# Kernel optimization log

Hardware: AMD Instinct MI355X
Metric: run time of the kernel (lower is better)

The kernel has to match this reference:

```python
import jax, jax.numpy as jnp
import numpy as np
from jax import lax

B, C, H, W = 8, 64, 256, 256
WSIZES = [8, 8]
DRATES = [1, 2]
SHIFT = True
CS = C // len(WSIZES)          # split channels = 32
SCALE = CS ** (-0.5)
EPS = 1e-6


def _ln2d(x, w, b):
    # channel-wise LayerNorm over dim 1 (biased variance), per LayerNormFunction
    mu = x.mean(1, keepdims=True)
    var = ((x - mu) ** 2).mean(1, keepdims=True)
    y = (x - mu) / jnp.sqrt(var + EPS)
    return w[None, :, None, None] * y + b[None, :, None, None]


def _conv1d(x, w, pad, dil):
    # x: [b, ci, L], w: [co, ci, k]
    return lax.conv_general_dilated(x, w, (1,), ((pad, pad),), rhs_dilation=(dil,),
                                    dimension_numbers=('NCH', 'OIH', 'NCH'))


def _eca(x, w1, w2, w3, wc):
    # x: [b,c,h,w] -> channel attention [b,c,1,1]
    y = x.mean((2, 3))[:, None, :]                      # [b,1,c]
    y1 = _conv1d(y, w1, 1, 1)
    y2 = _conv1d(y, w2, 2, 2)
    y3 = _conv1d(y, w3, 4, 4)
    y = _conv1d(jnp.concatenate([y1, y2, y3], axis=1), wc, 1, 1)  # [b,1,c]
    return jax.nn.sigmoid(jnp.transpose(y, (0, 2, 1))[..., None])  # [b,c,1,1]


def _conv1x1(x, w):
    # w: [co, ci]
    return jnp.einsum('bchw,oc->bohw', x, w)


def _win(x, ws):
    # [b,c,H,W] -> [(b nh nw), ws*ws, c]
    b, c, h, w = x.shape
    nh, nw = h // ws, w // ws
    x = x.reshape(b, c, nh, ws, nw, ws).transpose(0, 2, 4, 3, 5, 1)
    return x.reshape(b * nh * nw, ws * ws, c)


def _unwin(x, b, nh, nw, ws):
    c = x.shape[-1]
    x = x.reshape(b, nh, nw, ws, ws, c).transpose(0, 5, 1, 3, 2, 4)
    return x.reshape(b, c, nh * ws, nw * ws)


def setup_inputs() -> dict:
    key = jax.random.key(0)
    ks = jax.random.split(key, 16)
    g = lambda k, shape: jax.random.normal(k, shape, jnp.float32) * 0.02
    return {
        'x0': jax.random.normal(ks[0], (B, C, H, W), jnp.float32),
        'ln_w': jnp.ones((C,), jnp.float32),
        'ln_b': jnp.zeros((C,), jnp.float32),
        'dw_w': g(ks[1], (C, 1, 3, 3)),
        'dw_b': jnp.zeros((C,), jnp.float32),
        'eca_w1': g(ks[2], (1, 1, 3)),
        'eca_w2': g(ks[3], (1, 1, 3)),
        'eca_w3': g(ks[4], (1, 1, 3)),
        'eca_wc': g(ks[5], (1, 3, 3)),
        'wq': g(ks[6], (C, C)),
        'wk': g(ks[7], (C, C)),
        'wv': g(ks[8], (C, C)),
        'down_w': g(ks[9], (CS, 1, 2, 2)),
        'down_b': jnp.zeros((CS,), jnp.float32),
        'sa_w': g(ks[10], (1, C)),
        'sa_b': jnp.zeros((1,), jnp.float32),
        'po_w': g(ks[11], (C, C)),
        'po_b': jnp.zeros((C,), jnp.float32),
    }


def reference(x0, ln_w, ln_b, dw_w, dw_b, eca_w1, eca_w2, eca_w3, eca_wc,
              wq, wk, wv, down_w, down_b, sa_w, sa_b, po_w, po_b):
    b, c, h, w = x0.shape
    x = _ln2d(x0, ln_w, ln_b)
    # depthwise 3x3
    x1 = lax.conv_general_dilated(x, dw_w, (1, 1), ((1, 1), (1, 1)),
                                  feature_group_count=c,
                                  dimension_numbers=('NCHW', 'OIHW', 'NCHW'))
    x1 = x1 + dw_b[None, :, None, None]
    ca = _eca(x1, eca_w1, eca_w2, eca_w3, eca_wc)
    vs = jnp.split(_conv1x1(x, wv) * ca, len(WSIZES), axis=1)
    qs = jnp.split(_conv1x1(x, wq), len(WSIZES), axis=1)
    ks_ = jnp.split(_conv1x1(x, wk), len(WSIZES), axis=1)

    ys = []
    for idx in range(len(WSIZES)):
        ws = WSIZES[idx]
        ds = ws // DRATES[idx]
        q = qs[idx]
        if SHIFT:
            q = jnp.roll(q, (-ws // 2, -ws // 2), (2, 3))
        q = _win(q, ws)
        if DRATES[idx] != 1:
            # depthwise 2x2 stride-2 downsample of k, v
            def down(t):
                t = lax.conv_general_dilated(t, down_w, (2, 2), 'VALID',
                                             feature_group_count=CS,
                                             dimension_numbers=('NCHW', 'OIHW', 'NCHW'))
                return t + down_b[None, :, None, None]
            k = down(ks_[idx])
            v = down(vs[idx])
            if SHIFT:
                k = jnp.roll(k, (-ds // 2, -ds // 2), (2, 3))
                v = jnp.roll(v, (-ds // 2, -ds // 2), (2, 3))
            k = _win(k, ds)
            v = _win(v, ds)
        else:
            k, v = ks_[idx], vs[idx]
            if SHIFT:
                k = jnp.roll(k, (-ws // 2, -ws // 2), (2, 3))
                v = jnp.roll(v, (-ws // 2, -ws // 2), (2, 3))
            k = _win(k, ws)
            v = _win(v, ws)
        atn = jax.nn.softmax(jnp.einsum('nqc,nkc->nqk', q, k) * SCALE, axis=-1)
        y_ = jnp.einsum('nqk,nkc->nqc', atn, v)
        y_ = _unwin(y_, b, h // ws, w // ws, ws)
        if SHIFT:
            y_ = jnp.roll(y_, (ws // 2, ws // 2), (2, 3))
        ys.append(y_)

    y = jnp.concatenate(ys, axis=1)
    x1m = jax.nn.sigmoid(_conv1x1(y, sa_w) + sa_b[None, :, None, None]) * x1
    y = _conv1x1(y + x1m, po_w) + po_b[None, :, None, None]
    return y + x0
```

## Files before the change

kernel.cpp:

```cpp
#include <hip/hip_runtime.h>
#include <hip/hip_bf16.h>

using bf16 = __hip_bfloat16;

constexpr int B = 8, C = 64, H = 256, W = 256;
constexpr int HWs = H * W;
constexpr int NPIX = B * H * W;
constexpr long long NELEM = (long long)B * C * H * W;
constexpr int CS = 32;
constexpr int Hd = 128, Wd = 128;
constexpr int HWd = Hd * Wd;
constexpr int NDOWN = B * CS * HWd;
constexpr float EPS = 1e-6f;
constexpr float SCALE = 0.17677669529663687f;

typedef __attribute__((ext_vector_type(8))) short short8v;
typedef __attribute__((ext_vector_type(8))) unsigned short ushort8v;
typedef __attribute__((ext_vector_type(4))) unsigned short ushort4v;
typedef __attribute__((ext_vector_type(4))) float f32x4;

__device__ __forceinline__ float b2f(bf16 v) { return __bfloat162float(v); }
__device__ __forceinline__ bf16 f2b(float v) { return __float2bfloat16(v); }
__device__ __forceinline__ unsigned short f2bu(float v) {
  bf16 t = __float2bfloat16(v);
  unsigned short u;
  __builtin_memcpy(&u, &t, 2);
  return u;
}
__device__ __forceinline__ float bu2f(unsigned short u) {
  bf16 t;
  __builtin_memcpy(&t, &u, 2);
  return __bfloat162float(t);
}
__device__ __forceinline__ short8v pack2(ushort4v a, ushort4v b) {
  short8v r;
  r[0] = (short)a[0]; r[1] = (short)a[1]; r[2] = (short)a[2]; r[3] = (short)a[3];
  r[4] = (short)b[0]; r[5] = (short)b[1]; r[6] = (short)b[2]; r[7] = (short)b[3];
  return r;
}

__global__ __launch_bounds__(256) void qkv_ln_kernel(
    const float* __restrict__ x0, const float* __restrict__ lnw,
    const float* __restrict__ lnb, const float* __restrict__ wq,
    const float* __restrict__ wk, const float* __restrict__ wv,
    unsigned short* __restrict__ xo, unsigned short* __restrict__ q0,
    unsigned short* __restrict__ q1, unsigned short* __restrict__ k0,
    unsigned short* __restrict__ v0, unsigned short* __restrict__ ksp,
    unsigned short* __restrict__ vsp) {
  __shared__ unsigned short sA[4][2560];
  __shared__ unsigned short sB[4][2560];
  int lane = threadIdx.x & 63, wid = threadIdx.x >> 6;
  int lr = lane & 15, lg = lane >> 4;
  unsigned short* A = &sA[wid][0];
  unsigned short* Bs = &sB[wid][0];
  int seg = blockIdx.x * 4 + wid;
  int p0 = seg * 64;
  int b = p0 >> 16;
  int hw0 = p0 & (HWs - 1);
  int r = hw0 >> 8, col0 = hw0 & 255;
  float lwv[16], lbv[16];
#pragma unroll
  for (int ks = 0; ks < 2; ++ks)
#pragma unroll
    for (int j = 0; j < 8; ++j) {
      int c = ks * 32 + lg * 4 + (j & 3) + 16 * (j >> 2);
      lwv[ks * 8 + j] = lnw[c];
      lbv[ks * 8 + j] = lnb[c];
    }
  short8v bx[4][2];
#pragma unroll
  for (int st = 0; st < 4; ++st) {
    const float* xp = x0 + (size_t)b * C * HWs + hw0 + st * 16 + lr;
    float xv[16];
#pragma unroll
    for (int ks = 0; ks < 2; ++ks)
#pragma unroll
      for (int j = 0; j < 8; ++j) {
        int c = ks * 32 + lg * 4 + (j & 3) + 16 * (j >> 2);
        xv[ks * 8 + j] = xp[(size_t)c * HWs];
      }
    float s = 0.f, s2 = 0.f;
#pragma unroll
    for (int i = 0; i < 16; ++i) { s += xv[i]; s2 += xv[i] * xv[i]; }
    s += __shfl_xor(s, 16, 64); s += __shfl_xor(s, 32, 64);
    s2 += __shfl_xor(s2, 16, 64); s2 += __shfl_xor(s2, 32, 64);
    float mu = s * (1.f / 64);
    float var = s2 * (1.f / 64) - mu * mu;
    float rstd = rsqrtf(var + EPS);
#pragma unroll
    for (int ks = 0; ks < 2; ++ks)
#pragma unroll
      for (int j = 0; j < 8; ++j) {
        float xn = lwv[ks * 8 + j] * ((xv[ks * 8 + j] - mu) * rstd) + lbv[ks * 8 + j];
        bx[st][ks][j] = (short)f2bu(xn);
      }
  }
  int rr = (r - 4) & 255;
  int tokr = (rr & 7) * 8;
  int wrow = b * 1024 + (rr >> 3) * 32;
  auto win_store = [&](const unsigned short* src, unsigned short* dst) {
#pragma unroll
    for (int i = 0; i < 4; ++i) {
      int g = i * 4 + (lane >> 4);
      int tl = (lane >> 2) & 3, ch8 = lane & 3;
      int px = g * 4 + tl;
      int ccw = (col0 + px - 4) & 255;
      size_t wb = (size_t)(wrow + (ccw >> 3)) * 2048 +
                  (size_t)(tokr + (ccw & 7)) * 32 + ch8 * 8;
      ushort8v d = *(const ushort8v*)(src + px * 40 + ch8 * 8);
      *(ushort8v*)(dst + wb) = d;
    }
  };
  auto load_wfrag = [&](const float* wsrc, short8v wf[4][2]) {
#pragma unroll
    for (int mt = 0; mt < 4; ++mt)
#pragma unroll
      for (int ks = 0; ks < 2; ++ks) {
        int rowoff = (mt * 16 + lr) * 64 + ks * 32 + lg * 4;
        short8v t;
#pragma unroll
        for (int j = 0; j < 8; ++j) {
          int kj = (j & 3) + 16 * (j >> 2);
          t[j] = (short)f2bu(wsrc[rowoff + kj]);
        }
        wf[mt][ks] = t;
      }
  };
  f32x4 zero = {0.f, 0.f, 0.f, 0.f};
#pragma unroll
  for (int half = 0; half < 2; ++half) {
#pragma unroll
    for (int st = 0; st < 4; ++st) {
      int px = st * 16 + lr;
#pragma unroll
      for (int j = 0; j < 8; ++j) {
        int c = lg * 4 + (j & 3) + 16 * (j >> 2);
        Bs[c * 80 + px] = (unsigned short)bx[st][half][j];
      }
    }
#pragma unroll
    for (int i = 0; i < 4; ++i) {
      int ch = i * 8 + (lane >> 3), pxg = lane & 7;
      ushort8v d = *(const ushort8v*)(Bs + ch * 80 + pxg * 8);
      *(ushort8v*)(xo + ((size_t)b * 64 + half * 32 + ch) * HWs + hw0 + pxg * 8) = d;
    }
  }
  {
    short8v wf[4][2];
    load_wfrag(wq, wf);
#pragma unroll
    for (int st = 0; st < 4; ++st) {
      f32x4 acc[4];
#pragma unroll
      for (int mt = 0; mt < 4; ++mt) {
        acc[mt] = __builtin_amdgcn_mfma_f32_16x16x32_bf16(wf[mt][0], bx[st][0], zero, 0, 0, 0);
        acc[mt] = __builtin_amdgcn_mfma_f32_16x16x32_bf16(wf[mt][1], bx[st][1], acc[mt], 0, 0, 0);
      }
      int px = st * 16 + lr;
#pragma unroll
      for (int mt = 0; mt < 2; ++mt)
#pragma unroll
        for (int i = 0; i < 4; ++i)
          A[px * 40 + mt * 16 + lg * 4 + i] = f2bu(acc[mt][i]);
#pragma unroll
      for (int mt = 2; mt < 4; ++mt)
#pragma unroll
        for (int i = 0; i < 4; ++i)
          Bs[px * 40 + (mt - 2) * 16 + lg * 4 + i] = f2bu(acc[mt][i]);
    }
    win_store(A, q0);
    win_store(Bs, q1);
  }
  {
    short8v wf[4][2];
    load_wfrag(wk, wf);
#pragma unroll
    for (int st = 0; st < 4; ++st) {
      f32x4 acc[4];
#pragma unroll
      for (int mt = 0; mt < 4; ++mt) {
        acc[mt] = __builtin_amdgcn_mfma_f32_16x16x32_bf16(wf[mt][0], bx[st][0], zero, 0, 0, 0);
        acc[mt] = __builtin_amdgcn_mfma_f32_16x16x32_bf16(wf[mt][1], bx[st][1], acc[mt], 0, 0, 0);
      }
      int px = st * 16 + lr;
#pragma unroll
      for (int mt = 0; mt < 2; ++mt)
#pragma unroll
        for (int i = 0; i < 4; ++i)
          A[px * 40 + mt * 16 + lg * 4 + i] = f2bu(acc[mt][i]);
#pragma unroll
      for (int mt = 2; mt < 4; ++mt)
#pragma unroll
        for (int i = 0; i < 4; ++i)
          Bs[((mt - 2) * 16 + lg * 4 + i) * 80 + px] = f2bu(acc[mt][i]);
    }
    win_store(A, k0);
#pragma unroll
    for (int i = 0; i < 4; ++i) {
      int ch = i * 8 + (lane >> 3), pxg = lane & 7;
      ushort8v d = *(const ushort8v*)(Bs + ch * 80 + pxg * 8);
      *(ushort8v*)(ksp + ((size_t)b * 32 + ch) * HWs + hw0 + pxg * 8) = d;
    }
  }
  {
    short8v wf[4][2];
    load_wfrag(wv, wf);
#pragma unroll
    for (int st = 0; st < 4; ++st) {
      f32x4 acc[4];
#pragma unroll
      for (int mt = 0; mt < 4; ++mt) {
        acc[mt] = __builtin_amdgcn_mfma_f32_16x16x32_bf16(wf[mt][0], bx[st][0], zero, 0, 0, 0);
        acc[mt] = __builtin_amdgcn_mfma_f32_16x16x32_bf16(wf[mt][1], bx[st][1], acc[mt], 0, 0, 0);
      }
      int px = st * 16 + lr;
#pragma unroll
      for (int mt = 0; mt < 2; ++mt)
#pragma unroll
        for (int i = 0; i < 4; ++i)
          A[px * 40 + mt * 16 + lg * 4 + i] = f2bu(acc[mt][i]);
#pragma unroll
      for (int mt = 2; mt < 4; ++mt)
#pragma unroll
        for (int i = 0; i < 4; ++i)
          Bs[((mt - 2) * 16 + lg * 4 + i) * 80 + px] = f2bu(acc[mt][i]);
    }
    win_store(A, v0);
#pragma unroll
    for (int i = 0; i < 4; ++i) {
      int ch = i * 8 + (lane >> 3), pxg = lane & 7;
      ushort8v d = *(const ushort8v*)(Bs + ch * 80 + pxg * 8);
      *(ushort8v*)(vsp + ((size_t)b * 32 + ch) * HWs + hw0 + pxg * 8) = d;
    }
  }
}

__global__ __launch_bounds__(256) void dw_kernel(
    const unsigned short* __restrict__ x, const float* __restrict__ dww,
    const float* __restrict__ dwb, unsigned short* __restrict__ x1,
    float* __restrict__ pool) {
  int tid = threadIdx.x;
  int tx = tid & 15, ty = tid >> 4;
  int h = blockIdx.x * 16 + ty;
  int c = blockIdx.y, b = blockIdx.z;
  const unsigned short* xp = x + ((size_t)b * C + c) * HWs;
  float kk[9];
#pragma unroll
  for (int i = 0; i < 9; ++i) kk[i] = dww[c * 9 + i];
  int w0 = tx * 16;
  float acc[16];
  float bias = dwb[c];
#pragma unroll
  for (int i = 0; i < 16; ++i) acc[i] = bias;
#pragma unroll
  for (int dr = 0; dr < 3; ++dr) {
    int hh = h + dr - 1;
    if (hh < 0 || hh >= H) continue;
    const unsigned short* rp = xp + hh * W;
    ushort8v r0 = *(const ushort8v*)(rp + w0);
    ushort8v r1 = *(const ushort8v*)(rp + w0 + 8);
    float p[18];
    p[0] = (w0 > 0) ? bu2f(rp[w0 - 1]) : 0.f;
    p[17] = (w0 + 16 < W) ? bu2f(rp[w0 + 16]) : 0.f;
#pragma unroll
    for (int i = 0; i < 8; ++i) { p[1 + i] = bu2f(r0[i]); p[9 + i] = bu2f(r1[i]); }
    float k0 = kk[dr * 3], k1 = kk[dr * 3 + 1], k2 = kk[dr * 3 + 2];
#pragma unroll
    for (int i = 0; i < 16; ++i)
      acc[i] += k0 * p[i] + k1 * p[i + 1] + k2 * p[i + 2];
  }
  ushort8v o0, o1;
  float s = 0.f;
#pragma unroll
  for (int i = 0; i < 8; ++i) { o0[i] = f2bu(acc[i]); o1[i] = f2bu(acc[i + 8]); }
#pragma unroll
  for (int i = 0; i < 16; ++i) s += acc[i];
  size_t ob = ((size_t)b * C + c) * HWs + h * W + w0;
  *(ushort8v*)(x1 + ob) = o0;
  *(ushort8v*)(x1 + ob + 8) = o1;
#pragma unroll
  for (int off = 32; off > 0; off >>= 1) s += __shfl_down(s, off, 64);
  __shared__ float red[4];
  if ((tid & 63) == 0) red[tid >> 6] = s;
  __syncthreads();
  if (tid == 0) atomicAdd(&pool[b * C + c], red[0] + red[1] + red[2] + red[3]);
}

__global__ __launch_bounds__(512) void eca_kernel(
    const float* __restrict__ pool, const float* __restrict__ w1,
    const float* __restrict__ w2, const float* __restrict__ w3,
    const float* __restrict__ wc, float* __restrict__ ca) {
  int tid = threadIdx.x;
  int b = tid >> 6, c = tid & 63;
  __shared__ float m[8][64], t1[8][64], t2[8][64], t3[8][64];
  m[b][c] = pool[tid] * (1.f / HWs);
  __syncthreads();
  auto gm = [&](int cc) -> float { return (cc >= 0 && cc < 64) ? m[b][cc] : 0.f; };
  t1[b][c] = w1[0] * gm(c - 1) + w1[1] * gm(c) + w1[2] * gm(c + 1);
  t2[b][c] = w2[0] * gm(c - 2) + w2[1] * gm(c) + w2[2] * gm(c + 2);
  t3[b][c] = w3[0] * gm(c - 4) + w3[1] * gm(c) + w3[2] * gm(c + 4);
  __syncthreads();
  auto g1 = [&](int cc) -> float { return (cc >= 0 && cc < 64) ? t1[b][cc] : 0.f; };
  auto g2 = [&](int cc) -> float { return (cc >= 0 && cc < 64) ? t2[b][cc] : 0.f; };
  auto g3 = [&](int cc) -> float { return (cc >= 0 && cc < 64) ? t3[b][cc] : 0.f; };
  float z = 0.f;
#pragma unroll
  for (int k = 0; k < 3; ++k) {
    z += wc[0 * 3 + k] * g1(c + k - 1);
    z += wc[1 * 3 + k] * g2(c + k - 1);
    z += wc[2 * 3 + k] * g3(c + k - 1);
  }
  ca[tid] = 1.f / (1.f + __expf(-z));
}

__global__ __launch_bounds__(256) void down_kernel(
    const unsigned short* __restrict__ ksp, const unsigned short* __restrict__ vsp,
    const float* __restrict__ dw, const float* __restrict__ db,
    unsigned short* __restrict__ kdw, unsigned short* __restrict__ vdw) {
  int t = blockIdx.x * 256 + threadIdx.x;
  int wxd = t & 31, i = (t >> 5) & 127, c = (t >> 12) & 31, b = t >> 17;
  const unsigned short* kp = ksp + ((size_t)b * 32 + c) * HWs;
  const unsigned short* vp = vsp + ((size_t)b * 32 + c) * HWs;
  float w00 = dw[c * 4], w01 = dw[c * 4 + 1], w10 = dw[c * 4 + 2], w11 = dw[c * 4 + 3];
  float bias = db[c];
  int rowa = (2 * i) * W, rowb = rowa + W;
  int c0a = (8 * wxd + 4) & 255, c0b = (8 * wxd + 8) & 255;
  ushort4v ka0 = *(const ushort4v*)(kp + rowa + c0a);
  ushort4v ka1 = *(const ushort4v*)(kp + rowa + c0b);
  ushort4v kb0 = *(const ushort4v*)(kp + rowb + c0a);
  ushort4v kb1 = *(const ushort4v*)(kp + rowb + c0b);
  ushort4v va0 = *(const ushort4v*)(vp + rowa + c0a);
  ushort4v va1 = *(const ushort4v*)(vp + rowa + c0b);
  ushort4v vb0 = *(const ushort4v*)(vp + rowb + c0a);
  ushort4v vb1 = *(const ushort4v*)(vp + rowb + c0b);
  int rr = (i - 2) & 127;
  size_t winb = ((size_t)(b * 1024 + (rr >> 2) * 32 + wxd)) * 512;
  int tokrow = (rr & 3) * 4;
  ushort4v hk, hv;
#pragma unroll
  for (int tx = 0; tx < 4; ++tx) {
    float k00, k01, k10, k11, v00, v01, v10, v11;
    if (tx < 2) {
      k00 = bu2f(ka0[2 * tx]); k01 = bu2f(ka0[2 * tx + 1]);
      k10 = bu2f(kb0[2 * tx]); k11 = bu2f(kb0[2 * tx + 1]);
      v00 = bu2f(va0[2 * tx]); v01 = bu2f(va0[2 * tx + 1]);
      v10 = bu2f(vb0[2 * tx]); v11 = bu2f(vb0[2 * tx + 1]);
    } else {
      k00 = bu2f(ka1[2 * (tx - 2)]); k01 = bu2f(ka1[2 * (tx - 2) + 1]);
      k10 = bu2f(kb1[2 * (tx - 2)]); k11 = bu2f(kb1[2 * (tx - 2) + 1]);
      v00 = bu2f(va1[2 * (tx - 2)]); v01 = bu2f(va1[2 * (tx - 2) + 1]);
      v10 = bu2f(vb1[2 * (tx - 2)]); v11 = bu2f(vb1[2 * (tx - 2) + 1]);
    }
    hk[tx] = f2bu(w00 * k00 + w01 * k01 + w10 * k10 + w11 * k11 + bias);
    hv[tx] = f2bu(w00 * v00 + w01 * v01 + w10 * v10 + w11 * v11 + bias);
  }
  *(ushort4v*)(vdw + winb + (size_t)c * 16 + tokrow) = hv;
#pragma unroll
  for (int tx = 0; tx < 4; ++tx)
    kdw[winb + (size_t)(tokrow + tx) * 32 + c] = hk[tx];
}

__global__ __launch_bounds__(256) void attn0_kernel(
    const unsigned short* __restrict__ q0, const unsigned short* __restrict__ k0,
    const unsigned short* __restrict__ v0, const float* __restrict__ ca,
    unsigned short* __restrict__ y) {
  __shared__ unsigned short zs[4][32][72];
  int tid = threadIdx.x;
  int lane = tid & 63, wid = tid >> 6;
  int lr = lane & 15, lg = lane >> 4;
  int widx = blockIdx.x * 4 + wid;
  int b = widx >> 10;
  unsigned short* zw = &zs[wid][0][0];
  float cav[8];
#pragma unroll
  for (int mt = 0; mt < 2; ++mt)
#pragma unroll
    for (int r2 = 0; r2 < 4; ++r2)
      cav[mt * 4 + r2] = ca[b * 64 + mt * 16 + lg * 4 + r2];
  {
    const unsigned short* vp = v0 + (size_t)widx * 2048 + (size_t)lane * 32;
#pragma unroll
    for (int j2 = 0; j2 < 4; ++j2) {
      ushort8v vv = *(const ushort8v*)(vp + j2 * 8);
#pragma unroll
      for (int i = 0; i < 8; ++i) zw[(j2 * 8 + i) * 72 + lane] = vv[i];
    }
  }
  const unsigned short* kw = k0 + (size_t)widx * 2048;
  const unsigned short* qw = q0 + (size_t)widx * 2048;
  short8v kf[4], qf[4];
#pragma unroll
  for (int kt = 0; kt < 4; ++kt) {
    ushort4v a = *(const ushort4v*)(kw + (kt * 16 + lr) * 32 + lg * 4);
    ushort4v b2 = *(const ushort4v*)(kw + (kt * 16 + lr) * 32 + lg * 4 + 16);
    kf[kt] = pack2(a, b2);
  }
#pragma unroll
  for (int qt = 0; qt < 4; ++qt) {
    ushort4v a = *(const ushort4v*)(qw + (qt * 16 + lr) * 32 + lg * 4);
    ushort4v b2 = *(const ushort4v*)(qw + (qt * 16 + lr) * 32 + lg * 4 + 16);
    qf[qt] = pack2(a, b2);
  }
  __syncthreads();
  short8v va[2][2];
#pragma unroll
  for (int mt = 0; mt < 2; ++mt)
#pragma unroll
    for (int ck = 0; ck < 2; ++ck) {
      ushort4v a = *(const ushort4v*)&zw[(mt * 16 + lr) * 72 + ck * 32 + lg * 4];
      ushort4v b2 = *(const ushort4v*)&zw[(mt * 16 + lr) * 72 + ck * 32 + lg * 4 + 16];
      va[mt][ck] = pack2(a, b2);
    }
  f32x4 zero = {0.f, 0.f, 0.f, 0.f};
#pragma unroll
  for (int qt = 0; qt < 4; ++qt) {
    f32x4 st[4];
#pragma unroll
    for (int kt = 0; kt < 4; ++kt)
      st[kt] = __builtin_amdgcn_mfma_f32_16x16x32_bf16(kf[kt], qf[qt], zero, 0, 0, 0);
    float mx = -1e30f;
#pragma unroll
    for (int kt = 0; kt < 4; ++kt)
#pragma unroll
      for (int r2 = 0; r2 < 4; ++r2) mx = fmaxf(mx, st[kt][r2]);
    mx = fmaxf(mx, __shfl_xor(mx, 16, 64));
    mx = fmaxf(mx, __shfl_xor(mx, 32, 64));
    float sum = 0.f;
#pragma unroll
    for (int kt = 0; kt < 4; ++kt)
#pragma unroll
      for (int r2 = 0; r2 < 4; ++r2) {
        float e = __expf(SCALE * (st[kt][r2] - mx));
        st[kt][r2] = e;
        sum += e;
      }
    sum += __shfl_xor(sum, 16, 64);
    sum += __shfl_xor(sum, 32, 64);
    float inv = 1.f / sum;
    short8v pb[2];
#pragma unroll
    for (int ck = 0; ck < 2; ++ck)
#pragma unroll
      for (int j = 0; j < 8; ++j)
        pb[ck][j] = (short)f2bu(st[ck * 2 + (j >> 2)][j & 3]);
#pragma unroll
    for (int mt = 0; mt < 2; ++mt) {
      f32x4 yt = __builtin_amdgcn_mfma_f32_16x16x32_bf16(va[mt][0], pb[0], zero, 0, 0, 0);
      yt = __builtin_amdgcn_mfma_f32_16x16x32_bf16(va[mt][1], pb[1], yt, 0, 0, 0);
#pragma unroll
      for (int r2 = 0; r2 < 4; ++r2)
        zw[(mt * 16 + lg * 4 + r2) * 72 + qt * 16 + lr] = f2bu(yt[r2] * inv * cav[mt * 4 + r2]);
    }
  }
  __syncthreads();
  int widx0 = blockIdx.x * 4;
  int b0 = widx0 >> 10, wy0 = (widx0 >> 5) & 31, wxb = widx0 & 31;
#pragma unroll
  for (int pass = 0; pass < 4; ++pass) {
    int sub = tid & 3, pair = tid >> 2;
    int ch = pair & 31;
    int row = pass * 2 + (pair >> 5);
    ushort8v t8 = *(const ushort8v*)&zs[sub][ch][row * 8];
    int r2 = (wy0 * 8 + row + 4) & 255;
    int colb = wxb * 8 + 4 + sub * 8;
    size_t yb = ((size_t)b0 * C + ch) * HWs + (size_t)r2 * W;
    if (colb <= 248) {
      *(ushort8v*)(y + yb + colb) = t8;
    } else {
      ushort4v lo, hi;
#pragma unroll
      for (int i = 0; i < 4; ++i) { lo[i] = t8[i]; hi[i] = t8[4 + i]; }
      *(ushort4v*)(y + yb + 252) = lo;
      *(ushort4v*)(y + yb) = hi;
    }
  }
}

__global__ __launch_bounds__(256) void attn1_kernel(
    const unsigned short* __restrict__ q1, const unsigned short* __restrict__ kdw,
    const unsigned short* __restrict__ vdw, const float* __restrict__ ca,
    unsigned short* __restrict__ y) {
  __shared__ unsigned short zs[4][32][72];
  int tid = threadIdx.x;
  int lane = tid & 63, wid = tid >> 6;
  int lr = lane & 15, lg = lane >> 4;
  int widx = blockIdx.x * 4 + wid;
  int b = widx >> 10;
  unsigned short* zw = &zs[wid][0][0];
  float cav[8];
#pragma unroll
  for (int mt = 0; mt < 2; ++mt)
#pragma unroll
    for (int r2 = 0; r2 < 4; ++r2)
      cav[mt * 4 + r2] = ca[b * 64 + 32 + mt * 16 + lg * 4 + r2];
  short8v kfr;
  {
    ushort4v a = *(const ushort4v*)(kdw + (size_t)widx * 512 + lr * 32 + lg * 4);
    ushort4v b2 = *(const ushort4v*)(kdw + (size_t)widx * 512 + lr * 32 + lg * 4 + 16);
    kfr = pack2(a, b2);
  }
  short8v va[2];
#pragma unroll
  for (int mt = 0; mt < 2; ++mt) {
    ushort4v a = *(const ushort4v*)(vdw + (size_t)widx * 512 + (mt * 16 + lr) * 16 + lg * 4);
    short8v t;
#pragma unroll
    for (int i = 0; i < 4; ++i) { t[i] = (short)a[i]; t[4 + i] = 0; }
    va[mt] = t;
  }
  const unsigned short* qw = q1 + (size_t)widx * 2048;
  short8v qf[4];
#pragma unroll
  for (int qt = 0; qt < 4; ++qt) {
    ushort4v a = *(const ushort4v*)(qw + (qt * 16 + lr) * 32 + lg * 4);
    ushort4v b2 = *(const ushort4v*)(qw + (qt * 16 + lr) * 32 + lg * 4 + 16);
    qf[qt] = pack2(a, b2);
  }
  f32x4 zero = {0.f, 0.f, 0.f, 0.f};
#pragma unroll
  for (int qt = 0; qt < 4; ++qt) {
    f32x4 st = __builtin_amdgcn_mfma_f32_16x16x32_bf16(kfr, qf[qt], zero, 0, 0, 0);
    float mx = fmaxf(fmaxf(st[0], st[1]), fmaxf(st[2], st[3]));
    mx = fmaxf(mx, __shfl_xor(mx, 16, 64));
    mx = fmaxf(mx, __shfl_xor(mx, 32, 64));
    float sum = 0.f;
#pragma unroll
    for (int r2 = 0; r2 < 4; ++r2) {
      float e = __expf(SCALE * (st[r2] - mx));
      st[r2] = e;
      sum += e;
    }
    sum += __shfl_xor(sum, 16, 64);
    sum += __shfl_xor(sum, 32, 64);
    float inv = 1.f / sum;
    short8v pb;
#pragma unroll
    for (int j = 0; j < 4; ++j) { pb[j] = (short)f2bu(st[j]); pb[4 + j] = 0; }
#pragma unroll
    for (int mt = 0; mt < 2; ++mt) {
      f32x4 yt = __builtin_amdgcn_mfma_f32_16x16x32_bf16(va[mt], pb, zero, 0, 0, 0);
#pragma unroll
      for (int r2 = 0; r2 < 4; ++r2)
        zw[(mt * 16 + lg * 4 + r2) * 72 + qt * 16 + lr] = f2bu(yt[r2] * inv * cav[mt * 4 + r2]);
    }
  }
  __syncthreads();
  int widx0 = blockIdx.x * 4;
  int b0 = widx0 >> 10, wy0 = (widx0 >> 5) & 31, wxb = widx0 & 31;
#pragma unroll
  for (int pass = 0; pass < 4; ++pass) {
    int sub = tid & 3, pair = tid >> 2;
    int ch = pair & 31;
    int row = pass * 2 + (pair >> 5);
    ushort8v t8 = *(const ushort8v*)&zs[sub][ch][row * 8];
    int r2 = (wy0 * 8 + row + 4) & 255;
    int colb = wxb * 8 + 4 + sub * 8;
    size_t yb = ((size_t)b0 * C + 32 + ch) * HWs + (size_t)r2 * W;
    if (colb <= 248) {
      *(ushort8v*)(y + yb + colb) = t8;
    } else {
      ushort4v lo, hi;
#pragma unroll
      for (int i = 0; i < 4; ++i) { lo[i] = t8[i]; hi[i] = t8[4 + i]; }
      *(ushort4v*)(y + yb + 252) = lo;
      *(ushort4v*)(y + yb) = hi;
    }
  }
}

__global__ __launch_bounds__(256) void final_mfma_kernel(
    const unsigned short* __restrict__ y, const unsigned short* __restrict__ x1,
    const float* __restrict__ x0, const float* __restrict__ sa_w,
    const float* __restrict__ sa_b, const float* __restrict__ po_w,
    const float* __restrict__ po_b, float* __restrict__ out) {
  __shared__ unsigned short zs[64][72];
  __shared__ float part[4][64];
  __shared__ float sgs[64];
  int tid = threadIdx.x;
  int lane = tid & 63, wid = tid >> 6;
  int lr = lane & 15, lg = lane >> 4;
  short8v ap[4][2];
#pragma unroll
  for (int mt = 0; mt < 4; ++mt)
#pragma unroll
    for (int ks = 0; ks < 2; ++ks) {
      int rowoff = (mt * 16 + lr) * 64 + ks * 32 + lg * 4;
      short8v tt;
#pragma unroll
      for (int j = 0; j < 8; ++j) {
        int kj = (j & 3) + 16 * (j >> 2);
        tt[j] = (short)f2bu(po_w[rowoff + kj]);
      }
      ap[mt][ks] = tt;
    }
  int cc = tid >> 2, qx = (tid & 3) * 16;
  int blk = blockIdx.x;
  int p0 = blk * 64;
  int b = p0 >> 16, hw0 = p0 & (HWs - 1);
  size_t rbase = (size_t)b * C * HWs + (size_t)cc * HWs + hw0 + qx;
  ushort8v y0 = *(const ushort8v*)(y + rbase);
  ushort8v y1 = *(const ushort8v*)(y + rbase + 8);
  ushort8v a0 = *(const ushort8v*)(x1 + rbase);
  ushort8v a1 = *(const ushort8v*)(x1 + rbase + 8);
  *(ushort8v*)&zs[cc][qx] = y0;
  *(ushort8v*)&zs[cc][qx + 8] = y1;
  __syncthreads();
  {
    int p = tid & 63, qr = tid >> 6;
    float s = 0.f;
#pragma unroll
    for (int c2 = 0; c2 < 16; ++c2)
      s += sa_w[qr * 16 + c2] * bu2f(zs[qr * 16 + c2][p]);
    part[qr][p] = s;
  }
  __syncthreads();
  if (tid < 64) {
    float sd = part[0][tid] + part[1][tid] + part[2][tid] + part[3][tid] + sa_b[0];
    sgs[tid] = 1.f / (1.f + __expf(-sd));
  }
  __syncthreads();
  {
    ushort8v z0, z1;
#pragma unroll
    for (int i = 0; i < 8; ++i) {
      z0[i] = f2bu(bu2f(y0[i]) + sgs[qx + i] * bu2f(a0[i]));
      z1[i] = f2bu(bu2f(y1[i]) + sgs[qx + 8 + i] * bu2f(a1[i]));
    }
    *(ushort8v*)&zs[cc][qx] = z0;
    *(ushort8v*)&zs[cc][qx + 8] = z1;
  }
  __syncthreads();
  short8v bz[2];
#pragma unroll
  for (int ks = 0; ks < 2; ++ks) {
    short8v tt;
#pragma unroll
    for (int j = 0; j < 8; ++j) {
      int c2 = ks * 32 + lg * 4 + (j & 3) + 16 * (j >> 2);
      tt[j] = (short)zs[c2][wid * 16 + lr];
    }
    bz[ks] = tt;
  }
  f32x4 zero = {0.f, 0.f, 0.f, 0.f};
  f32x4 acc[4];
#pragma unroll
  for (int mt = 0; mt < 4; ++mt) {
    acc[mt] = __builtin_amdgcn_mfma_f32_16x16x32_bf16(ap[mt][0], bz[0], zero, 0, 0, 0);
    acc[mt] = __builtin_amdgcn_mfma_f32_16x16x32_bf16(ap[mt][1], bz[1], acc[mt], 0, 0, 0);
  }
  size_t pbase = (size_t)b * C * HWs + hw0 + wid * 16 + lr;
#pragma unroll
  for (int mt = 0; mt < 4; ++mt)
#pragma unroll
    for (int i = 0; i < 4; ++i) {
      int o = mt * 16 + lg * 4 + i;
      out[pbase + (size_t)o * HWs] = acc[mt][i] + po_b[o] + x0[pbase + (size_t)o * HWs];
    }
}

extern "C" void kernel_launch(void* const* d_in, const int* in_sizes, int n_in,
                              void* d_out, int out_size, void* d_ws, size_t ws_size,
                              hipStream_t stream) {
  const float* x0    = (const float*)d_in[0];
  const float* ln_w  = (const float*)d_in[1];
  const float* ln_b  = (const float*)d_in[2];
  const float* dw_w  = (const float*)d_in[3];
  const float* dw_b  = (const float*)d_in[4];
  const float* ew1   = (const float*)d_in[5];
  const float* ew2   = (const float*)d_in[6];
  const float* ew3   = (const float*)d_in[7];
  const float* ewc   = (const float*)d_in[8];
  const float* wq    = (const float*)d_in[9];
  const float* wk    = (const float*)d_in[10];
  const float* wv    = (const float*)d_in[11];
  const float* dwn_w = (const float*)d_in[12];
  const float* dwn_b = (const float*)d_in[13];
  const float* sa_w  = (const float*)d_in[14];
  const float* sa_b  = (const float*)d_in[15];
  const float* po_w  = (const float*)d_in[16];
  const float* po_b  = (const float*)d_in[17];
  float* out = (float*)d_out;

  char* ws = (char*)d_ws;
  const size_t NB = (size_t)NELEM * sizeof(bf16);
  const size_t NH = NB / 2;
  const size_t NDB = (size_t)NDOWN * sizeof(bf16);
  bf16* xbuf  = (bf16*)(ws);
  bf16* x1buf = (bf16*)(ws + NB);
  unsigned short* q0b  = (unsigned short*)(ws + 2 * NB);
  unsigned short* q1b  = (unsigned short*)(ws + 2 * NB + NH);
  unsigned short* k0b  = (unsigned short*)(ws + 3 * NB);
  unsigned short* v0b  = (unsigned short*)(ws + 3 * NB + NH);
  unsigned short* kspb = (unsigned short*)(ws + 4 * NB);
  unsigned short* vspb = (unsigned short*)(ws + 4 * NB + NH);
  unsigned short* kdwb = (unsigned short*)(ws + 5 * NB);
  unsigned short* vdwb = (unsigned short*)(ws + 5 * NB + NDB);
  float* pool = (float*)(ws + 5 * NB + 2 * NDB);
  float* cabuf = pool + B * C;
  bf16* ybuf = xbuf;

  hipMemsetAsync(pool, 0, B * C * sizeof(float), stream);
  qkv_ln_kernel<<<2048, 256, 0, stream>>>(x0, ln_w, ln_b, wq, wk, wv,
                                          (unsigned short*)xbuf, q0b, q1b, k0b, v0b,
                                          kspb, vspb);
  dw_kernel<<<dim3(16, C, B), 256, 0, stream>>>((const unsigned short*)xbuf, dw_w, dw_b,
                                                (unsigned short*)x1buf, pool);
  eca_kernel<<<1, 512, 0, stream>>>(pool, ew1, ew2, ew3, ewc, cabuf);
  down_kernel<<<4096, 256, 0, stream>>>(kspb, vspb, dwn_w, dwn_b, kdwb, vdwb);
  attn0_kernel<<<2048, 256, 0, stream>>>(q0b, k0b, v0b, cabuf, (unsigned short*)ybuf);
  attn1_kernel<<<2048, 256, 0, stream>>>(q1b, kdwb, vdwb, cabuf, (unsigned short*)ybuf);
  final_mfma_kernel<<<NPIX / 64, 256, 0, stream>>>((const unsigned short*)ybuf,
                                                   (const unsigned short*)x1buf, x0,
                                                   sa_w, sa_b, po_w, po_b, out);
}
```

Before: 368.3 us.

## Make final kernel persistent per-wave with register-direct MFMA operand loads

The final 1x1-conv kernel no longer stages y in shared memory behind several block barriers. Each wave now loads its MFMA B-operand straight from global memory into registers, computes the spatial-attention gate with a cross-lane shuffle reduction, and loops persistently over 16-pixel tiles in a fixed grid of 2048 blocks. This also loads the weight fragments once per wave instead of once per 64 pixels. The cost is that the global reads are scalar 2-byte loads strided by channel, so they coalesce only across 16 lanes rather than using 16-byte vector loads.

```diff
diff --git a/kernel.cpp b/kernel.cpp
--- a/kernel.cpp
+++ b/kernel.cpp
@@ -573,11 +573,7 @@
     const float* __restrict__ x0, const float* __restrict__ sa_w,
     const float* __restrict__ sa_b, const float* __restrict__ po_w,
     const float* __restrict__ po_b, float* __restrict__ out) {
-  __shared__ unsigned short zs[64][72];
-  __shared__ float part[4][64];
-  __shared__ float sgs[64];
-  int tid = threadIdx.x;
-  int lane = tid & 63, wid = tid >> 6;
+  int lane = threadIdx.x & 63, wid = threadIdx.x >> 6;
   int lr = lane & 15, lg = lane >> 4;
   short8v ap[4][2];
 #pragma unroll
@@ -593,69 +589,65 @@
       }
       ap[mt][ks] = tt;
     }
-  int cc = tid >> 2, qx = (tid & 3) * 16;
-  int blk = blockIdx.x;
-  int p0 = blk * 64;
-  int b = p0 >> 16, hw0 = p0 & (HWs - 1);
-  size_t rbase = (size_t)b * C * HWs + (size_t)cc * HWs + hw0 + qx;
-  ushort8v y0 = *(const ushort8v*)(y + rbase);
-  ushort8v y1 = *(const ushort8v*)(y + rbase + 8);
-  ushort8v a0 = *(const ushort8v*)(x1 + rbase);
-  ushort8v a1 = *(const ushort8v*)(x1 + rbase + 8);
-  *(ushort8v*)&zs[cc][qx] = y0;
-  *(ushort8v*)&zs[cc][qx + 8] = y1;
-  __syncthreads();
-  {
-    int p = tid & 63, qr = tid >> 6;
+  float swv[16];
+#pragma unroll
+  for (int ks = 0; ks < 2; ++ks)
+#pragma unroll
+    for (int j = 0; j < 8; ++j) {
+      int c = ks * 32 + lg * 4 + (j & 3) + 16 * (j >> 2);
+      swv[ks * 8 + j] = sa_w[c];
+    }
+  float pbv[16];
+#pragma unroll
+  for (int mt = 0; mt < 4; ++mt)
+#pragma unroll
+    for (int i = 0; i < 4; ++i)
+      pbv[mt * 4 + i] = po_b[mt * 16 + lg * 4 + i];
+  float sab = sa_b[0];
+  f32x4 zero = {0.f, 0.f, 0.f, 0.f};
+  const int NT = NPIX / 16;
+  for (int t = blockIdx.x * 4 + wid; t < NT; t += gridDim.x * 4) {
+    int p0 = t * 16;
+    int b = p0 >> 16, hw0 = p0 & (HWs - 1);
+    const unsigned short* yp = y + (size_t)b * C * HWs + hw0 + lr;
+    const unsigned short* xp = x1 + (size_t)b * C * HWs + hw0 + lr;
+    float yv[16], xv[16];
     float s = 0.f;
 #pragma unroll
-    for (int c2 = 0; c2 < 16; ++c2)
-      s += sa_w[qr * 16 + c2] * bu2f(zs[qr * 16 + c2][p]);
-    part[qr][p] = s;
-  }
-  __syncthreads();
-  if (tid < 64) {
-    float sd = part[0][tid] + part[1][tid] + part[2][tid] + part[3][tid] + sa_b[0];
-    sgs[tid] = 1.f / (1.f + __expf(-sd));
-  }
-  __syncthreads();
-  {
-    ushort8v z0, z1;
-#pragma unroll
-    for (int i = 0; i < 8; ++i) {
-      z0[i] = f2bu(bu2f(y0[i]) + sgs[qx + i] * bu2f(a0[i]));
-      z1[i] = f2bu(bu2f(y1[i]) + sgs[qx + 8 + i] * bu2f(a1[i]));
-    }
-    *(ushort8v*)&zs[cc][qx] = z0;
-    *(ushort8v*)&zs[cc][qx + 8] = z1;
-  }
-  __syncthreads();
-  short8v bz[2];
-#pragma unroll
-  for (int ks = 0; ks < 2; ++ks) {
-    short8v tt;
-#pragma unroll
-    for (int j = 0; j < 8; ++j) {
-      int c2 = ks * 32 + lg * 4 + (j & 3) + 16 * (j >> 2);
-      tt[j] = (short)zs[c2][wid * 16 + lr];
-    }
-    bz[ks] = tt;
-  }
-  f32x4 zero = {0.f, 0.f, 0.f, 0.f};
-  f32x4 acc[4];
-#pragma unroll
-  for (int mt = 0; mt < 4; ++mt) {
-    acc[mt] = __builtin_amdgcn_mfma_f32_16x16x32_bf16(ap[mt][0], bz[0], zero, 0, 0, 0);
-    acc[mt] = __builtin_amdgcn_mfma_f32_16x16x32_bf16(ap[mt][1], bz[1], acc[mt], 0, 0, 0);
-  }
-  size_t pbase = (size_t)b * C * HWs + hw0 + wid * 16 + lr;
-#pragma unroll
-  for (int mt = 0; mt < 4; ++mt)
-#pragma unroll
-    for (int i = 0; i < 4; ++i) {
-      int o = mt * 16 + lg * 4 + i;
-      out[pbase + (size_t)o * HWs] = acc[mt][i] + po_b[o] + x0[pbase + (size_t)o * HWs];
-    }
+    for (int ks = 0; ks < 2; ++ks)
+#pragma unroll
+      for (int j = 0; j < 8; ++j) {
+        int c = ks * 32 + lg * 4 + (j & 3) + 16 * (j >> 2);
+        int idx = ks * 8 + j;
+        yv[idx] = bu2f(yp[(size_t)c * HWs]);
+        xv[idx] = bu2f(xp[(size_t)c * HWs]);
+        s += swv[idx] * yv[idx];
+      }
+    s += __shfl_xor(s, 16, 64);
+    s += __shfl_xor(s, 32, 64);
+    float sg = 1.f / (1.f + __expf(-(s + sab)));
+    short8v bz[2];
+#pragma unroll
+    for (int ks = 0; ks < 2; ++ks)
+#pragma unroll
+      for (int j = 0; j < 8; ++j)
+        bz[ks][j] = (short)f2bu(yv[ks * 8 + j] + sg * xv[ks * 8 + j]);
+    f32x4 acc[4];
+#pragma unroll
+    for (int mt = 0; mt < 4; ++mt) {
+      acc[mt] = __builtin_amdgcn_mfma_f32_16x16x32_bf16(ap[mt][0], bz[0], zero, 0, 0, 0);
+      acc[mt] = __builtin_amdgcn_mfma_f32_16x16x32_bf16(ap[mt][1], bz[1], acc[mt], 0, 0, 0);
+    }
+    size_t pbase = (size_t)b * C * HWs + hw0 + lr;
+#pragma unroll
+    for (int mt = 0; mt < 4; ++mt)
+#pragma unroll
+      for (int i = 0; i < 4; ++i) {
+        int o = mt * 16 + lg * 4 + i;
+        size_t idx = pbase + (size_t)o * HWs;
+        out[idx] = acc[mt][i] + pbv[mt * 4 + i] + x0[idx];
+      }
+  }
 }
 
 extern "C" void kernel_launch(void* const* d_in, const int* in_sizes, int n_in,
@@ -709,7 +701,7 @@
   down_kernel<<<4096, 256, 0, stream>>>(kspb, vspb, dwn_w, dwn_b, kdwb, vdwb);
   attn0_kernel<<<2048, 256, 0, stream>>>(q0b, k0b, v0b, cabuf, (unsigned short*)ybuf);
   attn1_kernel<<<2048, 256, 0, stream>>>(q1b, kdwb, vdwb, cabuf, (unsigned short*)ybuf);
-  final_mfma_kernel<<<NPIX / 64, 256, 0, stream>>>((const unsigned short*)ybuf,
-                                                   (const unsigned short*)x1buf, x0,
-                                                   sa_w, sa_b, po_w, po_b, out);
-}
+  final_mfma_kernel<<<2048, 256, 0, stream>>>((const unsigned short*)ybuf,
+                                              (const unsigned short*)x1buf, x0,
+                                              sa_w, sa_b, po_w, po_b, out);
+}
```

Result: slower. 403.2 us (+9.5%).
